# Kernel tuning notes

Measured on AMD Instinct MI355X. Metric: run time of the kernel, lower is better.

## Reference

```python
import jax, jax.numpy as jnp
import numpy as np
from jax import lax

DIM = 256
NI, NS, NP = 8, 4, 16
H = W = 36
SCALE = 20.0
POOL = 4
EPS_BN = 1e-5


def setup_inputs() -> dict:
    key = jax.random.key(0)
    ks = jax.random.split(key, 20)
    feat = jax.random.normal(ks[0], (NI, NS, DIM, H, W), jnp.float32)
    # proposals in xywh; scaled by 20 inside PrRoIPool, so keep boxes inside the 36x36 map
    xy = jax.random.uniform(ks[1], (NI, NS, NP, 2), jnp.float32) * 1.2
    wh = 0.1 + jax.random.uniform(ks[2], (NI, NS, NP, 2), jnp.float32) * 0.4
    proposals = jnp.concatenate([xy, wh], axis=-1)

    def kaiming(k, shape, fan_in):
        return jax.random.normal(k, shape, jnp.float32) * np.float32(np.sqrt(2.0 / fan_in))

    d = dict(feat=feat, proposals=proposals)
    for i, name in enumerate(['conv1', 'conv2', 'conv3']):
        d[name + '_w'] = kaiming(ks[3 + i], (DIM, DIM, 3, 3), DIM * 9)
        d[name + '_b'] = jnp.zeros((DIM,), jnp.float32)
        d['bn%d_g' % (i + 1)] = jax.random.uniform(ks[6 + i], (DIM,), jnp.float32)
        d['bn%d_b' % (i + 1)] = jnp.zeros((DIM,), jnp.float32)
    d['fc_w'] = kaiming(ks[9], (DIM, DIM * POOL * POOL), DIM * POOL * POOL)
    d['fc_b'] = jnp.zeros((DIM,), jnp.float32)
    d['fcbn_g'] = jax.random.uniform(ks[10], (DIM,), jnp.float32)
    d['fcbn_b'] = jnp.zeros((DIM,), jnp.float32)
    d['iou_w'] = kaiming(ks[11], (1, DIM), DIM)
    d['iou_b'] = jnp.zeros((1,), jnp.float32)
    return d


def _cbr(x, w, b, g, beta):
    # Conv(3x3, pad 1) + BatchNorm (training-mode batch stats) + ReLU
    x = lax.conv_general_dilated(x, w, (1, 1), ((1, 1), (1, 1)),
                                 dimension_numbers=('NCHW', 'OIHW', 'NCHW'))
    x = x + b[None, :, None, None]
    m = x.mean((0, 2, 3), keepdims=True)
    v = x.var((0, 2, 3), keepdims=True)
    x = (x - m) / jnp.sqrt(v + EPS_BN) * g[None, :, None, None] + beta[None, :, None, None]
    return jax.nn.relu(x)


def _trapcum_last(a):
    # trapezoidal cumulative integral along last axis, value 0 at index 0
    mid = 0.5 * (a[..., :-1] + a[..., 1:])
    return jnp.concatenate([jnp.zeros_like(a[..., :1]), jnp.cumsum(mid, axis=-1)], axis=-1)


def _prroi_pool(feat, rois, pooled=POOL, scale=SCALE):
    # Precise RoI pooling: exact double integral of the bilinear interpolant per bin,
    # computed analytically via trapezoidal cumulative integrals of the feature map.
    N, C, Hh, Ww = feat.shape
    Ux = _trapcum_last(feat)                                            # int_0^x f
    Uy = jnp.swapaxes(_trapcum_last(jnp.swapaxes(feat, -1, -2)), -1, -2)  # int_0^y f
    T = jnp.swapaxes(_trapcum_last(jnp.swapaxes(Ux, -1, -2)), -1, -2)     # int_0^y int_0^x f

    b = rois[:, 0].astype(jnp.int32)
    x1, y1, x2, y2 = (rois[:, 1] * scale, rois[:, 2] * scale,
                      rois[:, 3] * scale, rois[:, 4] * scale)
    bw = (x2 - x1) / pooled
    bh = (y2 - y1) / pooled
    grid = jnp.arange(pooled + 1, dtype=feat.dtype)
    xs = jnp.clip(x1[:, None] + bw[:, None] * grid, 0.0, Ww - 1)        # (R, P+1)
    ys = jnp.clip(y1[:, None] + bh[:, None] * grid, 0.0, Hh - 1)
    wx = jnp.clip(jnp.floor(xs), 0, Ww - 2).astype(jnp.int32)
    hy = jnp.clip(jnp.floor(ys), 0, Hh - 2).astype(jnp.int32)
    sx = xs - wx.astype(feat.dtype)
    sy = ys - hy.astype(feat.dtype)
    px1 = 0.5 * sx * sx
    px0 = sx - px1
    py1 = 0.5 * sy * sy
    py0 = sy - py1

    def g(arr, hi, wi):
        # gather per-RoI values -> (R, P+1, P+1, C), rows index y, cols index x
        return arr[b[:, None, None], :, hi[:, :, None], wi[:, None, :]]

    px0e = px0[:, None, :, None]
    px1e = px1[:, None, :, None]
    py0e = py0[:, :, None, None]
    py1e = py1[:, :, None, None]
    h0, h1 = hy, hy + 1
    w0, w1 = wx, wx + 1
    # antiderivative G(X, Y) = int_0^Y int_0^X f of the bilinear interpolant
    G = (g(T, h0, w0)
         + g(Uy, h0, w0) * px0e + g(Uy, h0, w1) * px1e
         + py0e * (g(Ux, h0, w0) + g(feat, h0, w0) * px0e + g(feat, h0, w1) * px1e)
         + py1e * (g(Ux, h1, w0) + g(feat, h1, w0) * px0e + g(feat, h1, w1) * px1e))
    # per-bin integral via inclusion-exclusion on the (P+1)x(P+1) corner grid
    d = G[:, 1:, 1:] - G[:, :-1, 1:] - G[:, 1:, :-1] + G[:, :-1, :-1]   # (R, P, P, C)
    area = (bw * bh)[:, None, None, None]
    out = jnp.where(area > 1e-8, d / jnp.maximum(area, 1e-8), 0.0)
    return jnp.transpose(out, (0, 3, 1, 2))  # (R, C, P, P)


def reference(feat, proposals, conv1_w, conv1_b, bn1_g, bn1_b, conv2_w, conv2_b,
              bn2_g, bn2_b, conv3_w, conv3_b, bn3_g, bn3_b, fc_w, fc_b,
              fcbn_g, fcbn_b, iou_w, iou_b):
    ni, ns = proposals.shape[0], proposals.shape[1]
    x = feat.reshape(-1, *feat.shape[-3:])
    x = _cbr(x, conv1_w, conv1_b, bn1_g, bn1_b)
    x = _cbr(x, conv2_w, conv2_b, bn2_g, bn2_b)
    x = _cbr(x, conv3_w, conv3_b, bn3_g, bn3_b)

    props = proposals.reshape(ni * ns, -1, 4)
    B, P = props.shape[0], props.shape[1]
    xyxy = jnp.concatenate([props[..., 0:2], props[..., 0:2] + props[..., 2:4]], axis=-1)
    bidx = jnp.broadcast_to(jnp.arange(B, dtype=props.dtype)[:, None, None], (B, P, 1))
    rois = jnp.concatenate([bidx, xyxy], axis=-1).reshape(-1, 5)

    rf = _prroi_pool(x, rois)                       # (B*P, C, 4, 4)
    fcx = rf.reshape(rf.shape[0], -1) @ fc_w.T + fc_b
    m = fcx.mean(0)
    v = fcx.var(0)
    fcx = jax.nn.relu((fcx - m) / jnp.sqrt(v + EPS_BN) * fcbn_g + fcbn_b)
    iou = fcx @ iou_w.T + iou_b                     # (B*P, 1)
    return iou.reshape(ni, ns, -1)
```

## Files before the change

### kernel.cpp

```cpp
#include <hip/hip_runtime.h>
#include <hip/hip_bf16.h>
#include <stdint.h>

#define CDIM 256
#define HH 36
#define WW 36
#define NPX 1296
#define PW 38
#define PPIX 1444
#define NIMG 32
#define NROI 512
#define FCK 4096
#define EPS_BN 1e-5f
#define SBLK 192
#define NWC (9*CDIM*CDIM)

typedef __bf16 bf16;
typedef __bf16 bf16x8 __attribute__((ext_vector_type(8)));
typedef float f32x4 __attribute__((ext_vector_type(4)));
typedef unsigned short us8 __attribute__((ext_vector_type(8)));

#define GLD16(g, l) __builtin_amdgcn_global_load_lds( \
    (__attribute__((address_space(1))) void*)(g),     \
    (__attribute__((address_space(3))) void*)(l), 16, 0, 0)

__global__ void k_prep(const float* __restrict__ w0, const float* __restrict__ w1,
                       const float* __restrict__ w2, const float* __restrict__ fcw,
                       bf16* __restrict__ wb, bf16* __restrict__ fwb) {
  int i = blockIdx.x * 256 + threadIdx.x;
  if (i < 3 * NWC) {
    int l = i / NWC, r = i - l * NWC;
    const float* ws = (l == 0) ? w0 : (l == 1) ? w1 : w2;
    int tap = r / (CDIM * CDIM);
    int rem = r - tap * (CDIM * CDIM);
    int co = rem >> 8, ci = rem & 255;
    wb[i] = (bf16)ws[(size_t)(co * CDIM + ci) * 9 + tap];
  } else {
    int j = i - 3 * NWC;
    if (j < CDIM * FCK) fwb[j] = (bf16)fcw[j];
  }
}

__global__ void k_convert(const float* __restrict__ feat, bf16* __restrict__ xp) {
  __shared__ bf16 tile[CDIM * 38];
  int h = blockIdx.x, n = blockIdx.y, t = threadIdx.x;
  const float* src = feat + (size_t)n * CDIM * NPX + (size_t)h * WW;
#pragma unroll 4
  for (int i = 0; i < 36; ++i) {
    int f = i * 256 + t;
    int c = (int)(((unsigned)f * 7282u) >> 18);
    int w = f - c * 36;
    tile[c * 38 + w] = (bf16)src[(size_t)c * NPX + w];
  }
  __syncthreads();
  bf16* dst = xp + (size_t)n * PPIX * CDIM + ((h + 1) * PW + 1) * CDIM + t;
#pragma unroll 4
  for (int w = 0; w < 36; ++w) dst[w * CDIM] = tile[t * 38 + w];
}

__global__ __launch_bounds__(256) void k_conv(
    const bf16* __restrict__ xp, const bf16* __restrict__ wb,
    bf16* __restrict__ y)
{
  __shared__ __align__(16) bf16 ldsA[2][4096];
  __shared__ __align__(16) bf16 ldsB[2][4096];
  const int tid = threadIdx.x;
  const int wave = tid >> 6, lane = tid & 63;

  const int B = blockIdx.x;
  const int xcd = B & 7, idx = B >> 3;
  const int ng = idx / 22, inner = idx - ng * 22;
  const int n = (ng << 3) + xcd;
  const int cot = inner / 11, pxt = inner - cot * 11;

  const int q = lane >> 2;
  const int gsw = (lane & 3) ^ ((q >> 1) & 3);
  const int rA = wave * 32 + q;
  const bf16* aS0 = wb + (size_t)(cot * 128 + rA) * CDIM + gsw * 8;
  const bf16* aS1 = aS0 + 16 * CDIM;
  int pxa = pxt * 128 + rA;       if (pxa > NPX - 1) pxa = NPX - 1;
  int pxb = pxt * 128 + rA + 16;  if (pxb > NPX - 1) pxb = NPX - 1;
  const int ha = pxa / 36, wa = pxa - ha * 36;
  const int hb = pxb / 36, wbv = pxb - hb * 36;
  const bf16* bS0 = xp + (size_t)n * (PPIX * CDIM) + ((ha + 1) * PW + (wa + 1)) * CDIM + gsw * 8;
  const bf16* bS1 = xp + (size_t)n * (PPIX * CDIM) + ((hb + 1) * PW + (wbv + 1)) * CDIM + gsw * 8;

  const int fr = lane & 15, fg = lane >> 4;
  const int fsw = (fg ^ ((fr >> 1) & 3)) * 8;
  const int wco = wave >> 1, wpx = wave & 1;
  const int aoff = (wco * 64 + fr) * 32 + fsw;
  const int boff = (wpx * 64 + fr) * 32 + fsw;

  f32x4 acc[4][4];
#pragma unroll
  for (int i = 0; i < 4; ++i)
#pragma unroll
    for (int j = 0; j < 4; ++j) acc[i][j] = f32x4{0.f, 0.f, 0.f, 0.f};

  {
    const int xoff = -(PW + 1) * CDIM;
    GLD16(aS0, &ldsA[0][wave * 1024]);
    GLD16(aS1, &ldsA[0][wave * 1024 + 512]);
    GLD16(bS0 + xoff, &ldsB[0][wave * 1024]);
    GLD16(bS1 + xoff, &ldsB[0][wave * 1024 + 512]);
  }

#pragma unroll 2
  for (int k = 0; k < 72; ++k) {
    const int buf = k & 1;
    __syncthreads();
    if (k + 1 < 72) {
      const int kn = k + 1;
      const int tap = kn >> 3, ci0 = (kn & 7) << 5;
      const int dh = tap / 3 - 1, dw = tap - (tap / 3) * 3 - 1;
      const int woff = tap * (CDIM * CDIM) + ci0;
      const int xoff = (dh * PW + dw) * CDIM + ci0;
      const int nb = buf ^ 1;
      GLD16(aS0 + woff, &ldsA[nb][wave * 1024]);
      GLD16(aS1 + woff, &ldsA[nb][wave * 1024 + 512]);
      GLD16(bS0 + xoff, &ldsB[nb][wave * 1024]);
      GLD16(bS1 + xoff, &ldsB[nb][wave * 1024 + 512]);
    }
    bf16x8 av[4], bv[4];
#pragma unroll
    for (int i = 0; i < 4; ++i) av[i] = *(const bf16x8*)&ldsA[buf][aoff + i * 512];
#pragma unroll
    for (int j = 0; j < 4; ++j) bv[j] = *(const bf16x8*)&ldsB[buf][boff + j * 512];
#pragma unroll
    for (int i = 0; i < 4; ++i)
#pragma unroll
      for (int j = 0; j < 4; ++j)
        acc[i][j] = __builtin_amdgcn_mfma_f32_16x16x32_bf16(av[i], bv[j], acc[i][j], 0, 0, 0);
  }

#pragma unroll
  for (int j = 0; j < 4; ++j) {
    const int px = pxt * 128 + wpx * 64 + j * 16 + fr;
    if (px < NPX) {
      bf16* dst = y + ((size_t)n * NPX + px) * CDIM + cot * 128 + wco * 64 + fg * 4;
#pragma unroll
      for (int i = 0; i < 4; ++i) {
        f32x4 a = acc[i][j];
        union { bf16 b4[4]; ushort4 u4; } pk;
        pk.b4[0] = (bf16)a[0]; pk.b4[1] = (bf16)a[1];
        pk.b4[2] = (bf16)a[2]; pk.b4[3] = (bf16)a[3];
        *(ushort4*)(dst + i * 16) = pk.u4;
      }
    }
  }
}

__global__ void k_statsb(const bf16* __restrict__ y, float* __restrict__ psum,
                         float* __restrict__ psq) {
  __shared__ float lsum[8][256];
  __shared__ float lsq[8][256];
  int t = threadIdx.x;
  int c8 = (t & 31) * 8, rg = t >> 5;
  size_t row0 = (size_t)blockIdx.x * 216 + rg;
  float s[8], qq[8];
#pragma unroll
  for (int k = 0; k < 8; ++k) { s[k] = 0.f; qq[k] = 0.f; }
  for (int i = 0; i < 27; ++i) {
    const bf16* p = y + (row0 + (size_t)i * 8) * CDIM + c8;
    union { bf16 b8[8]; us8 u; } v;
    v.u = *(const us8*)p;
#pragma unroll
    for (int k = 0; k < 8; ++k) {
      float f = (float)v.b8[k];
      s[k] += f; qq[k] += f * f;
    }
  }
#pragma unroll
  for (int k = 0; k < 8; ++k) { lsum[rg][c8 + k] = s[k]; lsq[rg][c8 + k] = qq[k]; }
  __syncthreads();
  float ss = 0.f, sq2 = 0.f;
#pragma unroll
  for (int g = 0; g < 8; ++g) { ss += lsum[g][t]; sq2 += lsq[g][t]; }
  psum[blockIdx.x * 256 + t] = ss;
  psq[blockIdx.x * 256 + t] = sq2;
}

__global__ void k_sredfin(const float* __restrict__ psum, const float* __restrict__ psq,
                          const float* __restrict__ g, const float* __restrict__ b,
                          float* __restrict__ sc, float* __restrict__ sh, float invn) {
  int c = threadIdx.x;
  float s = 0.f, q = 0.f;
  for (int i = 0; i < SBLK; ++i) { s += psum[i * 256 + c]; q += psq[i * 256 + c]; }
  float m = s * invn;
  float v = q * invn - m * m;
  float sca = g[c] * rsqrtf(v + EPS_BN);
  sc[c] = sca;
  sh[c] = b[c] - m * sca;
}

__global__ void k_normalize(const bf16* __restrict__ y, const float* __restrict__ sc,
                            const float* __restrict__ sh, bf16* __restrict__ xp) {
  int t = threadIdx.x;
  int n = blockIdx.y;
  int px = blockIdx.x * 8 + (t >> 5);
  int c8 = (t & 31) * 8;
  const bf16* srcp = y + ((size_t)n * NPX + px) * CDIM + c8;
  union { bf16 b8[8]; us8 u; } in, outp;
  in.u = *(const us8*)srcp;
  int h = px / 36, w = px - h * 36;
#pragma unroll
  for (int i = 0; i < 8; ++i) {
    float v = (float)in.b8[i];
    outp.b8[i] = (bf16)fmaxf(v * sc[c8 + i] + sh[c8 + i], 0.f);
  }
  *(us8*)(xp + (size_t)n * PPIX * CDIM + ((h + 1) * PW + (w + 1)) * CDIM + c8) = outp.u;
}

__device__ __forceinline__ float hatH(float u) {
  u = fminf(fmaxf(u, -1.f), 1.f);
  float p = u + 1.f;
  return (u < 0.f) ? 0.5f * p * p : 0.5f + u * (1.f - 0.5f * u);
}

__global__ __launch_bounds__(128) void k_pool(
    const bf16* __restrict__ y, const float* __restrict__ sc,
    const float* __restrict__ sh, const float* __restrict__ props,
    bf16* __restrict__ rf) {
  int roi = blockIdx.x;
  int c = blockIdx.y * 128 + threadIdx.x;
  int b = roi >> 4;
  const float* pr = props + (size_t)roi * 4;
  float x1 = pr[0] * 20.f, yy1 = pr[1] * 20.f;
  float x2 = (pr[0] + pr[2]) * 20.f, yy2 = (pr[1] + pr[3]) * 20.f;
  float bw = (x2 - x1) * 0.25f, bh = (yy2 - yy1) * 0.25f;

  float xs[5], ys[5];
#pragma unroll
  for (int j = 0; j < 5; ++j) {
    xs[j] = fminf(fmaxf(x1 + bw * j, 0.f), 35.f);
    ys[j] = fminf(fmaxf(yy1 + bh * j, 0.f), 35.f);
  }
  float wxv[4][5], wyv[4][5];
  int sx[4], sy[4];
#pragma unroll
  for (int j = 0; j < 4; ++j) {
    float a = xs[j], bb = xs[j + 1];
    int s = (int)floorf(a);
    sx[j] = s;
#pragma unroll
    for (int k = 0; k < 5; ++k) {
      float w = (float)(s + k);
      wxv[j][k] = hatH(bb - w) - hatH(a - w);
    }
    float ay = ys[j], by = ys[j + 1];
    int t = (int)floorf(ay);
    sy[j] = t;
#pragma unroll
    for (int k = 0; k < 5; ++k) {
      float w = (float)(t + k);
      wyv[j][k] = hatH(by - w) - hatH(ay - w);
    }
  }

  float s_ = sc[c], t_ = sh[c];
  const bf16* yb = y + (size_t)b * NPX * CDIM + c;
  float acc[4][4];
#pragma unroll
  for (int i = 0; i < 4; ++i)
#pragma unroll
    for (int j = 0; j < 4; ++j) acc[i][j] = 0.f;

#pragma unroll
  for (int i = 0; i < 4; ++i) {
#pragma unroll
    for (int ky = 0; ky < 5; ++ky) {
      float wy = wyv[i][ky];
      if (wy == 0.f) continue;
      int h = sy[i] + ky; if (h > 35) h = 35;
      const bf16* rowp = yb + h * (WW * CDIM);
#pragma unroll
      for (int j = 0; j < 4; ++j) {
        float rd = 0.f;
#pragma unroll
        for (int kx = 0; kx < 5; ++kx) {
          int w = sx[j] + kx; if (w > 35) w = 35;
          float f = fmaxf((float)rowp[w * CDIM] * s_ + t_, 0.f);
          rd += wxv[j][kx] * f;
        }
        acc[i][j] += wy * rd;
      }
    }
  }

  float area = bw * bh;
  float inv = area > 1e-8f ? 1.f / area : 0.f;
  bf16 outv[16];
#pragma unroll
  for (int i = 0; i < 4; ++i)
#pragma unroll
    for (int j = 0; j < 4; ++j)
      outv[i * 4 + j] = (bf16)(acc[i][j] * inv);
  bf16* dst = rf + (size_t)roi * FCK + c * 16;
  *(us8*)(dst)     = *(us8*)&outv[0];
  *(us8*)(dst + 8) = *(us8*)&outv[8];
}

__global__ __launch_bounds__(256) void k_fcgemm(const bf16* __restrict__ rf,
                                                const bf16* __restrict__ fw,
                                                float* __restrict__ fcp) {
  int tid = threadIdx.x, wave = tid >> 6, lane = tid & 63;
  int wo = wave >> 1, wr = wave & 1;
  int rt = blockIdx.x, ot = blockIdx.y, ks = blockIdx.z;
  int fr = lane & 15, fg = lane >> 4;
  const bf16* ap = fw + (size_t)(ot * 64 + wo * 32 + fr) * FCK + ks * 512 + fg * 8;
  const bf16* bp = rf + (size_t)(rt * 64 + wr * 32 + fr) * FCK + ks * 512 + fg * 8;
  f32x4 acc[2][2];
#pragma unroll
  for (int i = 0; i < 2; ++i)
#pragma unroll
    for (int j = 0; j < 2; ++j) acc[i][j] = f32x4{0.f, 0.f, 0.f, 0.f};
#pragma unroll 4
  for (int k = 0; k < 512; k += 32) {
    bf16x8 a0 = *(const bf16x8*)(ap + k);
    bf16x8 a1 = *(const bf16x8*)(ap + 16 * FCK + k);
    bf16x8 b0 = *(const bf16x8*)(bp + k);
    bf16x8 b1 = *(const bf16x8*)(bp + 16 * FCK + k);
    acc[0][0] = __builtin_amdgcn_mfma_f32_16x16x32_bf16(a0, b0, acc[0][0], 0, 0, 0);
    acc[0][1] = __builtin_amdgcn_mfma_f32_16x16x32_bf16(a0, b1, acc[0][1], 0, 0, 0);
    acc[1][0] = __builtin_amdgcn_mfma_f32_16x16x32_bf16(a1, b0, acc[1][0], 0, 0, 0);
    acc[1][1] = __builtin_amdgcn_mfma_f32_16x16x32_bf16(a1, b1, acc[1][1], 0, 0, 0);
  }
#pragma unroll
  for (int i = 0; i < 2; ++i)
#pragma unroll
    for (int j = 0; j < 2; ++j) {
      int o = ot * 64 + wo * 32 + i * 16 + fg * 4;
      int r = rt * 64 + wr * 32 + j * 16 + fr;
      *(f32x4*)(fcp + ((size_t)ks * NROI + r) * CDIM + o) = acc[i][j];
    }
}

__global__ void k_fcred(const float* __restrict__ fcp, float* __restrict__ fcx) {
  int r = blockIdx.x, o = threadIdx.x;
  float s = 0.f;
#pragma unroll
  for (int ks = 0; ks < 8; ++ks) s += fcp[((size_t)ks * NROI + r) * CDIM + o];
  fcx[(size_t)r * CDIM + o] = s;
}

__global__ void k_fcstatfin(const float* __restrict__ fcx, const float* __restrict__ g,
                            const float* __restrict__ b, float* __restrict__ sc,
                            float* __restrict__ sh) {
  int c = threadIdx.x;
  float s = 0.f, q = 0.f;
  for (int r = 0; r < NROI; ++r) {
    float v = fcx[(size_t)r * CDIM + c];
    s += v; q += v * v;
  }
  float m = s * (1.f / 512.f);
  float vv = q * (1.f / 512.f) - m * m;
  float sca = g[c] * rsqrtf(vv + EPS_BN);
  sc[c] = sca;
  sh[c] = b[c] - m * sca;
}

__global__ void k_iou(const float* __restrict__ fcx, const float* __restrict__ sc,
                      const float* __restrict__ sh, const float* __restrict__ iw,
                      const float* __restrict__ ib, float* __restrict__ out) {
  __shared__ float red[4];
  int roi = blockIdx.x, t = threadIdx.x;
  float v = fcx[(size_t)roi * CDIM + t];
  v = fmaxf(v * sc[t] + sh[t], 0.f) * iw[t];
#pragma unroll
  for (int o = 32; o > 0; o >>= 1) v += __shfl_down(v, o);
  if ((t & 63) == 0) red[t >> 6] = v;
  __syncthreads();
  if (t == 0) out[roi] = red[0] + red[1] + red[2] + red[3] + ib[0];
}

extern "C" void kernel_launch(void* const* d_in, const int* in_sizes, int n_in,
                              void* d_out, int out_size, void* d_ws, size_t ws_size,
                              hipStream_t stream) {
  (void)in_sizes; (void)n_in; (void)out_size;
  const float* feat  = (const float*)d_in[0];
  const float* props = (const float*)d_in[1];
  const float* convw[3] = {(const float*)d_in[2], (const float*)d_in[6], (const float*)d_in[10]};
  const float* bng[3]   = {(const float*)d_in[4], (const float*)d_in[8], (const float*)d_in[12]};
  const float* bnb[3]   = {(const float*)d_in[5], (const float*)d_in[9], (const float*)d_in[13]};
  const float* fcw  = (const float*)d_in[14];
  const float* fcg  = (const float*)d_in[16];
  const float* fcbb = (const float*)d_in[17];
  const float* iw   = (const float*)d_in[18];
  const float* ib   = (const float*)d_in[19];
  float* out = (float*)d_out;

  char* w = (char*)d_ws;
  size_t off = 0;
  auto take = [&](size_t sz) -> char* { char* p = w + off; off += (sz + 255) & ~(size_t)255; return p; };
  const size_t SZ_XP = (size_t)NIMG * PPIX * CDIM * 2;
  const size_t SZ_YB = (size_t)NIMG * NPX * CDIM * 2;
  const size_t SZ_P  = (size_t)SBLK * 256 * 4;
  bf16*  xp0 = (bf16*)take(SZ_XP);
  bf16*  xp1 = (bf16*)take(SZ_XP);
  bf16*  y   = (bf16*)take(SZ_YB);
  bf16*  wball = (bf16*)take((size_t)3 * NWC * 2);
  bf16*  fwb = (bf16*)take((size_t)CDIM * FCK * 2);
  bf16*  rfb = (bf16*)take((size_t)NROI * FCK * 2);
  float* fcx = (float*)take((size_t)NROI * CDIM * 4);
  float* fcp = (float*)take((size_t)8 * NROI * CDIM * 4);
  float* psum = (float*)take(SZ_P);
  float* psq  = (float*)take(SZ_P);
  float* scsh = (float*)take(8 * 256 * 4);
  if (off > ws_size) return;

  hipMemsetAsync(xp0, 0, SZ_XP * 2, stream);

  k_prep<<<dim3((3 * NWC + CDIM * FCK + 255) / 256), 256, 0, stream>>>(
      convw[0], convw[1], convw[2], fcw, wball, fwb);
  k_convert<<<dim3(HH, NIMG), 256, 0, stream>>>(feat, xp0);

  for (int l = 0; l < 3; ++l) {
    bf16* xin = (l == 1) ? xp1 : xp0;
    bf16* wbl = wball + (size_t)l * NWC;
    k_conv<<<dim3(704), 256, 0, stream>>>(xin, wbl, y);
    k_statsb<<<dim3(SBLK), 256, 0, stream>>>(y, psum, psq);
    float* sc = scsh + l * 512; float* sh = sc + 256;
    k_sredfin<<<dim3(1), 256, 0, stream>>>(psum, psq, bng[l], bnb[l], sc, sh, 1.f / 41472.f);
    if (l < 2) {
      bf16* xo = (l == 0) ? xp1 : xp0;
      k_normalize<<<dim3(NPX / 8, NIMG), 256, 0, stream>>>(y, sc, sh, xo);
    }
  }
  float* sc3 = scsh + 2 * 512; float* sh3 = sc3 + 256;
  k_pool<<<dim3(NROI, 2), 128, 0, stream>>>(y, sc3, sh3, props, rfb);
  k_fcgemm<<<dim3(8, 4, 8), 256, 0, stream>>>(rfb, fwb, fcp);
  k_fcred<<<dim3(NROI), 256, 0, stream>>>(fcp, fcx);
  float* fsc = scsh + 3 * 512; float* fsh = fsc + 256;
  k_fcstatfin<<<dim3(1), 256, 0, stream>>>(fcx, fcg, fcbb, fsc, fsh);
  k_iou<<<dim3(NROI), 256, 0, stream>>>(fcx, fsc, fsh, iw, ib, out);
}
```

Measured before the change: 462.0 us.

## Zero only halo borders and widen parallelism in stats, pooling and BN reductions

```diff
diff --git a/kernel.cpp b/kernel.cpp
--- a/kernel.cpp
+++ b/kernel.cpp
@@ -12,7 +12,7 @@
 #define NROI 512
 #define FCK 4096
 #define EPS_BN 1e-5f
-#define SBLK 192
+#define SBLK 324
 #define NWC (9*CDIM*CDIM)
 
 typedef __bf16 bf16;
@@ -23,6 +23,26 @@
 #define GLD16(g, l) __builtin_amdgcn_global_load_lds( \
     (__attribute__((address_space(1))) void*)(g),     \
     (__attribute__((address_space(3))) void*)(l), 16, 0, 0)
+
+__global__ void k_halo(bf16* __restrict__ xp0, bf16* __restrict__ xp1) {
+  int n = blockIdx.x, a = blockIdx.y, t = threadIdx.x;
+  bf16* base = (a ? xp1 : xp0) + (size_t)n * PPIX * CDIM;
+  us8 z = {0, 0, 0, 0, 0, 0, 0, 0};
+  for (int i = t; i < (2 * PW * CDIM) / 8; i += 256) {
+    int half = (PW * CDIM) / 8;
+    int row = (i < half) ? 0 : 37;
+    int off = (i < half) ? i : i - half;
+    *(us8*)(base + (size_t)row * PW * CDIM + off * 8) = z;
+  }
+  for (int i = t; i < (2 * 36 * CDIM) / 8; i += 256) {
+    int half = (36 * CDIM) / 8;
+    int side = (i < half) ? 0 : 37;
+    int j = (i < half) ? i : i - half;
+    int h = 1 + (j >> 5);
+    int cv = j & 31;
+    *(us8*)(base + ((size_t)h * PW + side) * CDIM + cv * 8) = z;
+  }
+}
 
 __global__ void k_prep(const float* __restrict__ w0, const float* __restrict__ w1,
                        const float* __restrict__ w2, const float* __restrict__ fcw,
@@ -156,11 +176,11 @@
   __shared__ float lsq[8][256];
   int t = threadIdx.x;
   int c8 = (t & 31) * 8, rg = t >> 5;
-  size_t row0 = (size_t)blockIdx.x * 216 + rg;
+  size_t row0 = (size_t)blockIdx.x * 128 + rg;
   float s[8], qq[8];
 #pragma unroll
   for (int k = 0; k < 8; ++k) { s[k] = 0.f; qq[k] = 0.f; }
-  for (int i = 0; i < 27; ++i) {
+  for (int i = 0; i < 16; ++i) {
     const bf16* p = y + (row0 + (size_t)i * 8) * CDIM + c8;
     union { bf16 b8[8]; us8 u; } v;
     v.u = *(const us8*)p;
@@ -180,17 +200,26 @@
   psq[blockIdx.x * 256 + t] = sq2;
 }
 
-__global__ void k_sredfin(const float* __restrict__ psum, const float* __restrict__ psq,
-                          const float* __restrict__ g, const float* __restrict__ b,
-                          float* __restrict__ sc, float* __restrict__ sh, float invn) {
-  int c = threadIdx.x;
+__global__ __launch_bounds__(1024) void k_sredfin(
+    const float* __restrict__ psum, const float* __restrict__ psq,
+    const float* __restrict__ g, const float* __restrict__ b,
+    float* __restrict__ sc, float* __restrict__ sh, float invn) {
+  __shared__ float ls[4][256], lq[4][256];
+  int t = threadIdx.x;
+  int c = t & 255, gi = t >> 8;
   float s = 0.f, q = 0.f;
-  for (int i = 0; i < SBLK; ++i) { s += psum[i * 256 + c]; q += psq[i * 256 + c]; }
-  float m = s * invn;
-  float v = q * invn - m * m;
-  float sca = g[c] * rsqrtf(v + EPS_BN);
-  sc[c] = sca;
-  sh[c] = b[c] - m * sca;
+  for (int i = gi; i < SBLK; i += 4) { s += psum[i * 256 + c]; q += psq[i * 256 + c]; }
+  ls[gi][c] = s; lq[gi][c] = q;
+  __syncthreads();
+  if (gi == 0) {
+    s = ls[0][c] + ls[1][c] + ls[2][c] + ls[3][c];
+    q = lq[0][c] + lq[1][c] + lq[2][c] + lq[3][c];
+    float m = s * invn;
+    float v = q * invn - m * m;
+    float sca = g[c] * rsqrtf(v + EPS_BN);
+    sc[c] = sca;
+    sh[c] = b[c] - m * sca;
+  }
 }
 
 __global__ void k_normalize(const bf16* __restrict__ y, const float* __restrict__ sc,
@@ -223,20 +252,18 @@
     bf16* __restrict__ rf) {
   int roi = blockIdx.x;
   int c = blockIdx.y * 128 + threadIdx.x;
+  int i0 = blockIdx.z * 2;
   int b = roi >> 4;
   const float* pr = props + (size_t)roi * 4;
   float x1 = pr[0] * 20.f, yy1 = pr[1] * 20.f;
   float x2 = (pr[0] + pr[2]) * 20.f, yy2 = (pr[1] + pr[3]) * 20.f;
   float bw = (x2 - x1) * 0.25f, bh = (yy2 - yy1) * 0.25f;
 
-  float xs[5], ys[5];
-#pragma unroll
-  for (int j = 0; j < 5; ++j) {
-    xs[j] = fminf(fmaxf(x1 + bw * j, 0.f), 35.f);
-    ys[j] = fminf(fmaxf(yy1 + bh * j, 0.f), 35.f);
-  }
-  float wxv[4][5], wyv[4][5];
-  int sx[4], sy[4];
+  float xs[5];
+#pragma unroll
+  for (int j = 0; j < 5; ++j) xs[j] = fminf(fmaxf(x1 + bw * j, 0.f), 35.f);
+  float wxv[4][5];
+  int sx[4];
 #pragma unroll
   for (int j = 0; j < 4; ++j) {
     float a = xs[j], bb = xs[j + 1];
@@ -247,31 +274,37 @@
       float w = (float)(s + k);
       wxv[j][k] = hatH(bb - w) - hatH(a - w);
     }
-    float ay = ys[j], by = ys[j + 1];
-    int t = (int)floorf(ay);
-    sy[j] = t;
+  }
+  float wyv[2][5];
+  int sy[2];
+#pragma unroll
+  for (int ii = 0; ii < 2; ++ii) {
+    float ay = fminf(fmaxf(yy1 + bh * (i0 + ii), 0.f), 35.f);
+    float by = fminf(fmaxf(yy1 + bh * (i0 + ii + 1), 0.f), 35.f);
+    int tt = (int)floorf(ay);
+    sy[ii] = tt;
 #pragma unroll
     for (int k = 0; k < 5; ++k) {
-      float w = (float)(t + k);
-      wyv[j][k] = hatH(by - w) - hatH(ay - w);
+      float w = (float)(tt + k);
+      wyv[ii][k] = hatH(by - w) - hatH(ay - w);
     }
   }
 
   float s_ = sc[c], t_ = sh[c];
   const bf16* yb = y + (size_t)b * NPX * CDIM + c;
-  float acc[4][4];
-#pragma unroll
-  for (int i = 0; i < 4; ++i)
-#pragma unroll
-    for (int j = 0; j < 4; ++j) acc[i][j] = 0.f;
-
-#pragma unroll
-  for (int i = 0; i < 4; ++i) {
+  float acc[2][4];
+#pragma unroll
+  for (int ii = 0; ii < 2; ++ii)
+#pragma unroll
+    for (int j = 0; j < 4; ++j) acc[ii][j] = 0.f;
+
+#pragma unroll
+  for (int ii = 0; ii < 2; ++ii) {
 #pragma unroll
     for (int ky = 0; ky < 5; ++ky) {
-      float wy = wyv[i][ky];
+      float wy = wyv[ii][ky];
       if (wy == 0.f) continue;
-      int h = sy[i] + ky; if (h > 35) h = 35;
+      int h = sy[ii] + ky; if (h > 35) h = 35;
       const bf16* rowp = yb + h * (WW * CDIM);
 #pragma unroll
       for (int j = 0; j < 4; ++j) {
@@ -282,22 +315,21 @@
           float f = fmaxf((float)rowp[w * CDIM] * s_ + t_, 0.f);
           rd += wxv[j][kx] * f;
         }
-        acc[i][j] += wy * rd;
+        acc[ii][j] += wy * rd;
       }
     }
   }
 
   float area = bw * bh;
   float inv = area > 1e-8f ? 1.f / area : 0.f;
-  bf16 outv[16];
-#pragma unroll
-  for (int i = 0; i < 4; ++i)
+  bf16 outv[8];
+#pragma unroll
+  for (int ii = 0; ii < 2; ++ii)
 #pragma unroll
     for (int j = 0; j < 4; ++j)
-      outv[i * 4 + j] = (bf16)(acc[i][j] * inv);
-  bf16* dst = rf + (size_t)roi * FCK + c * 16;
-  *(us8*)(dst)     = *(us8*)&outv[0];
-  *(us8*)(dst + 8) = *(us8*)&outv[8];
+      outv[ii * 4 + j] = (bf16)(acc[ii][j] * inv);
+  bf16* dst = rf + (size_t)roi * FCK + c * 16 + i0 * 4;
+  *(us8*)dst = *(us8*)&outv[0];
 }
 
 __global__ __launch_bounds__(256) void k_fcgemm(const bf16* __restrict__ rf,
@@ -343,20 +375,27 @@
   fcx[(size_t)r * CDIM + o] = s;
 }
 
-__global__ void k_fcstatfin(const float* __restrict__ fcx, const float* __restrict__ g,
-                            const float* __restrict__ b, float* __restrict__ sc,
-                            float* __restrict__ sh) {
-  int c = threadIdx.x;
+__global__ __launch_bounds__(1024) void k_fcstatfin(
+    const float* __restrict__ fcx, const float* __restrict__ g,
+    const float* __restrict__ b, float* __restrict__ sc, float* __restrict__ sh) {
+  __shared__ float ls[4][256], lq[4][256];
+  int t = threadIdx.x, c = t & 255, gi = t >> 8;
   float s = 0.f, q = 0.f;
-  for (int r = 0; r < NROI; ++r) {
+  for (int r = gi; r < NROI; r += 4) {
     float v = fcx[(size_t)r * CDIM + c];
     s += v; q += v * v;
   }
-  float m = s * (1.f / 512.f);
-  float vv = q * (1.f / 512.f) - m * m;
-  float sca = g[c] * rsqrtf(vv + EPS_BN);
-  sc[c] = sca;
-  sh[c] = b[c] - m * sca;
+  ls[gi][c] = s; lq[gi][c] = q;
+  __syncthreads();
+  if (gi == 0) {
+    s = ls[0][c] + ls[1][c] + ls[2][c] + ls[3][c];
+    q = lq[0][c] + lq[1][c] + lq[2][c] + lq[3][c];
+    float m = s * (1.f / 512.f);
+    float vv = q * (1.f / 512.f) - m * m;
+    float sca = g[c] * rsqrtf(vv + EPS_BN);
+    sc[c] = sca;
+    sh[c] = b[c] - m * sca;
+  }
 }
 
 __global__ void k_iou(const float* __restrict__ fcx, const float* __restrict__ sc,
@@ -408,8 +447,7 @@
   float* scsh = (float*)take(8 * 256 * 4);
   if (off > ws_size) return;
 
-  hipMemsetAsync(xp0, 0, SZ_XP * 2, stream);
-
+  k_halo<<<dim3(NIMG, 2), 256, 0, stream>>>(xp0, xp1);
   k_prep<<<dim3((3 * NWC + CDIM * FCK + 255) / 256), 256, 0, stream>>>(
       convw[0], convw[1], convw[2], fcw, wball, fwb);
   k_convert<<<dim3(HH, NIMG), 256, 0, stream>>>(feat, xp0);
@@ -420,17 +458,17 @@
     k_conv<<<dim3(704), 256, 0, stream>>>(xin, wbl, y);
     k_statsb<<<dim3(SBLK), 256, 0, stream>>>(y, psum, psq);
     float* sc = scsh + l * 512; float* sh = sc + 256;
-    k_sredfin<<<dim3(1), 256, 0, stream>>>(psum, psq, bng[l], bnb[l], sc, sh, 1.f / 41472.f);
+    k_sredfin<<<dim3(1), 1024, 0, stream>>>(psum, psq, bng[l], bnb[l], sc, sh, 1.f / 41472.f);
     if (l < 2) {
       bf16* xo = (l == 0) ? xp1 : xp0;
       k_normalize<<<dim3(NPX / 8, NIMG), 256, 0, stream>>>(y, sc, sh, xo);
     }
   }
   float* sc3 = scsh + 2 * 512; float* sh3 = sc3 + 256;
-  k_pool<<<dim3(NROI, 2), 128, 0, stream>>>(y, sc3, sh3, props, rfb);
+  k_pool<<<dim3(NROI, 2, 2), 128, 0, stream>>>(y, sc3, sh3, props, rfb);
   k_fcgemm<<<dim3(8, 4, 8), 256, 0, stream>>>(rfb, fwb, fcp);
   k_fcred<<<dim3(NROI), 256, 0, stream>>>(fcp, fcx);
   float* fsc = scsh + 3 * 512; float* fsh = fsc + 256;
-  k_fcstatfin<<<dim3(1), 256, 0, stream>>>(fcx, fcg, fcbb, fsc, fsh);
+  k_fcstatfin<<<dim3(1), 1024, 0, stream>>>(fcx, fcg, fcbb, fsc, fsh);
   k_iou<<<dim3(NROI), 256, 0, stream>>>(fcx, fsc, fsh, iw, ib, out);
 }
```

Result: slower. 513.9 us (+11.2%).
